# Performance work log

Measured on AMD Instinct MI355X. Metric: run time of the kernel, lower is better.

The kernel has to match this reference:

```python
import jax, jax.numpy as jnp
import numpy as np

N_NODES = 50000
N_EDGES = 800000
DIM = 128


def setup_inputs() -> dict:
    key = jax.random.key(0)
    k_x, k_e, k_w1, k_w2 = jax.random.split(key, 4)
    x = jax.random.normal(k_x, (N_NODES, DIM), dtype=jnp.float32)
    edge_index = jax.random.randint(k_e, (2, N_EDGES), 0, N_NODES, dtype=jnp.int64)
    scale = 1.0 / np.sqrt(DIM)
    W1 = jax.random.normal(k_w1, (DIM, DIM), dtype=jnp.float32) * scale
    b1 = jnp.zeros((DIM,), dtype=jnp.float32)
    W2 = jax.random.normal(k_w2, (DIM, DIM), dtype=jnp.float32) * scale
    b2 = jnp.zeros((DIM,), dtype=jnp.float32)
    return {"x": x, "edge_index": edge_index, "W1": W1, "b1": b1, "W2": W2, "b2": b2}


def _gcn_conv(x, W, b, src, dst, n_nodes):
    """PyG GCNConv: D^{-1/2}(A+I)D^{-1/2} (x @ W) + b, self-loops added."""
    h = x @ W  # [N, D]
    ones = jnp.ones(src.shape[0], dtype=h.dtype)
    # degree of A+I, counting incoming edges at target nodes plus self-loop
    deg = jax.ops.segment_sum(ones, dst, num_segments=n_nodes) + 1.0
    dinv = jax.lax.rsqrt(deg)  # [N]
    norm = dinv[src] * dinv[dst]  # [E]
    msgs = h[src] * norm[:, None]  # [E, D] gather (memory-bound)
    agg = jax.ops.segment_sum(msgs, dst, num_segments=n_nodes)  # scatter-add
    agg = agg + h * (dinv * dinv)[:, None]  # self-loop contribution
    return agg + b


def reference(x, edge_index, W1, b1, W2, b2):
    src, dst = edge_index[0], edge_index[1]
    n = x.shape[0]
    identity = x
    out = jax.nn.relu(_gcn_conv(x, W1, b1, src, dst, n))
    out = _gcn_conv(out, W2, b2, src, dst, n)
    return jax.nn.relu(out + identity)
```

## Files before the change

### kernel.cpp

```cpp
#include <hip/hip_runtime.h>

#define N_NODES 50000
#define N_EDGES 800000
#define DIM 128
#define NB 391
#define CAP 2560
#define NCH 7
#define BIN_CHUNK 4096
#define BIN_BLOCKS 196
#define GEMM_TILES 782
#define AGG_TILES 782
#define NPANEL 4

typedef unsigned int uint;
typedef unsigned short ushort;
typedef __attribute__((ext_vector_type(8))) __bf16 bf16x8;
typedef __attribute__((ext_vector_type(4))) float f32x4;

__device__ __forceinline__ uint f2bf(float f) {
    uint u = __float_as_uint(f);
    return (u + 0x7FFFu + ((u >> 16) & 1u)) >> 16;
}
__device__ __forceinline__ float2 bf2f2(uint u) {
    return make_float2(__uint_as_float(u << 16), __uint_as_float(u & 0xFFFF0000u));
}


__global__ __launch_bounds__(256) void prep_kernel(const float* __restrict__ W1,
                                                   const float* __restrict__ W2,
                                                   uint* __restrict__ Wt1,
                                                   uint* __restrict__ Wt2,
                                                   int* __restrict__ bincursor) {
    int idx = blockIdx.x * 256 + threadIdx.x;
    if (idx < 16384) {
        const float* W = (idx < 8192) ? W1 : W2;
        uint* Wt = (idx < 8192) ? Wt1 : Wt2;
        int i = idx & 8191;
        int n = i >> 6, k2 = i & 63;
        Wt[i] = f2bf(W[(2 * k2) * DIM + n]) | (f2bf(W[(2 * k2 + 1) * DIM + n]) << 16);
    } else {
        int b = idx - 16384;
        if (b < NB) bincursor[b] = b * CAP;
    }
}



__device__ __forceinline__ void gemm_tile64(const float* __restrict__ X,
                                            const uint* __restrict__ Wt, int base,
                                            uint* __restrict__ HP) {
    int t = threadIdx.x;
    int wv = t >> 6;
    int l = t & 63;
    int col = l & 15;
    int g = l >> 4;
    int grow = base + wv * 16 + col;
    int ar = grow > N_NODES - 1 ? N_NODES - 1 : grow;

    bf16x8 af[4];
    const float4* Xr = (const float4*)(X + (size_t)ar * DIM);
#pragma unroll
    for (int kk = 0; kk < 4; ++kk) {
        float4 x0 = Xr[kk * 8 + g * 2];
        float4 x1 = Xr[kk * 8 + g * 2 + 1];
        uint4 p;
        p.x = f2bf(x0.x) | (f2bf(x0.y) << 16);
        p.y = f2bf(x0.z) | (f2bf(x0.w) << 16);
        p.z = f2bf(x1.x) | (f2bf(x1.y) << 16);
        p.w = f2bf(x1.z) | (f2bf(x1.w) << 16);
        af[kk] = __builtin_bit_cast(bf16x8, p);
    }

    const uint4* Wr = (const uint4*)Wt;
    f32x4 acc[8];
#pragma unroll
    for (int n = 0; n < 8; ++n) acc[n] = (f32x4){0.f, 0.f, 0.f, 0.f};

#pragma unroll
    for (int n = 0; n < 8; ++n) {
        const uint4* wrow = Wr + (size_t)(n * 16 + col) * 16;
#pragma unroll
        for (int kk = 0; kk < 4; ++kk) {
            bf16x8 bf = __builtin_bit_cast(bf16x8, wrow[kk * 4 + g]);
            acc[n] = __builtin_amdgcn_mfma_f32_16x16x32_bf16(af[kk], bf, acc[n], 0, 0, 0);
        }
    }

    ushort* Hp = (ushort*)HP;
#pragma unroll
    for (int j = 0; j < 4; ++j) {
        int row = base + wv * 16 + g * 4 + j;
        if (row < N_NODES) {
#pragma unroll
            for (int n = 0; n < 8; ++n) {
                Hp[((size_t)((n >> 1) * N_NODES + row)) * 32 + (n & 1) * 16 + col] =
                    (ushort)f2bf(acc[n][j]);
            }
        }
    }
}


__global__ __launch_bounds__(256) void bin_gemm1_kernel(const int* __restrict__ ei,
                                                        int* __restrict__ bincursor,
                                                        uint* __restrict__ pairs,
                                                        const float* __restrict__ x,
                                                        const uint* __restrict__ Wt1,
                                                        uint* __restrict__ HP) {
    if (blockIdx.x >= BIN_BLOCKS) {
        gemm_tile64(x, Wt1, (blockIdx.x - BIN_BLOCKS) * 64, HP);
        return;
    }
    __shared__ int lh[NB];
    __shared__ int lbase[NB];
    int t = threadIdx.x;
    int eb = blockIdx.x * BIN_CHUNK;

    for (int b = t; b < NB; b += 256) lh[b] = 0;
    __syncthreads();

    int s_reg[16], d_reg[16];
#pragma unroll
    for (int i = 0; i < 16; ++i) {
        int e = eb + i * 256 + t;
        if (e < N_EDGES) {
            s_reg[i] = ei[e];
            d_reg[i] = ei[N_EDGES + e];
            atomicAdd(&lh[d_reg[i] >> 7], 1);
        } else {
            d_reg[i] = -1;
        }
    }
    __syncthreads();

    for (int b = t; b < NB; b += 256) {
        int c = lh[b];
        lbase[b] = c ? atomicAdd(&bincursor[b], c) : 0;
    }
    __syncthreads();
    for (int b = t; b < NB; b += 256) lh[b] = 0;
    __syncthreads();

#pragma unroll
    for (int i = 0; i < 16; ++i) {
        int d = d_reg[i];
        if (d >= 0) {
            int bin = d >> 7;
            int r = atomicAdd(&lh[bin], 1);
            pairs[lbase[bin] + r] = ((uint)s_reg[i] << 7) | (uint)(d & 127);
        }
    }
}


__global__ __launch_bounds__(256) void fill2_kernel(const uint* __restrict__ pairs,
                                                    const int* __restrict__ bincursor,
                                                    int* __restrict__ rowbeg,
                                                    int* __restrict__ rowend,
                                                    float* __restrict__ dinv,
                                                    int* __restrict__ csr_src) {
    __shared__ int cnt[128 * 8];
    __shared__ int nsum[128];
    __shared__ int nbase[128];
    int t = threadIdx.x;
    int blk = blockIdx.x;
    int bs = blk * CAP;
    int be = bincursor[blk];

    for (int i = t; i < 128 * 8; i += 256) cnt[i] = 0;
    __syncthreads();

    for (int p = bs + t; p < be; p += 256) {
        uint pr = pairs[p];
        atomicAdd(&cnt[(pr & 127u) * 8 + (pr >> 20)], 1);
    }
    __syncthreads();

    if (t < 128) {
        int s = 0;
#pragma unroll
        for (int c = 0; c < NCH; ++c) s += cnt[t * 8 + c];
        nsum[t] = s;
        nbase[t] = s;
    }
    __syncthreads();
#pragma unroll
    for (int off = 1; off < 128; off <<= 1) {
        int v = (t < 128 && t >= off) ? nbase[t - off] : 0;
        __syncthreads();
        if (t < 128) nbase[t] += v;
        __syncthreads();
    }

    if (t < 128) {
        int ex = nbase[t] - nsum[t];
        int node = blk * 128 + t;
        if (node < N_NODES) {
            rowbeg[node] = bs + ex;
            rowend[node] = bs + nbase[t];
            dinv[node] = rsqrtf((float)nsum[t] + 1.0f);
        }
        int run = ex;
#pragma unroll
        for (int c = 0; c < NCH; ++c) {
            int v = cnt[t * 8 + c];
            cnt[t * 8 + c] = run;
            run += v;
        }
    }
    __syncthreads();

    for (int p = bs + t; p < be; p += 256) {
        uint pr = pairs[p];
        int r = atomicAdd(&cnt[(pr & 127u) * 8 + (pr >> 20)], 1);
        csr_src[bs + r] = (int)(pr >> 7);
    }
}


template <bool DSRC, bool OBF>
__global__ __launch_bounds__(256) void aggP_kernel(const int* __restrict__ rowbeg,
                                                   const int* __restrict__ rowend,
                                                   const int* __restrict__ csr_src,
                                                   const uint* __restrict__ HP,
                                                   const float* __restrict__ dinv,
                                                   const float* __restrict__ bias,
                                                   const float* __restrict__ resid,
                                                   void* __restrict__ outv) {
    int bid = blockIdx.x;
    int panel = bid & 3;
    int tile = bid >> 2;
    int t = threadIdx.x;
    int wv = t >> 6;
    int l = t & 63;
    int sub = l >> 2;
    int li = l & 3;
    int node = tile * 64 + wv * 16 + sub;
    bool valid = node < N_NODES;
    int nn = valid ? node : N_NODES - 1;

    int beg = rowbeg[nn];
    int end = valid ? rowend[nn] : beg;
    float di = dinv[nn];

    const uint4* H = (const uint4*)HP + (size_t)panel * (N_NODES * 4);

    float a0, a1, a2, a3, a4, a5, a6, a7;
    {
        uint4 su = H[(size_t)nn * 4 + li];
        float2 v0 = bf2f2(su.x), v1 = bf2f2(su.y), v2 = bf2f2(su.z), v3 = bf2f2(su.w);
        float sf = DSRC ? di : 1.0f;
        a0 = sf * v0.x; a1 = sf * v0.y; a2 = sf * v1.x; a3 = sf * v1.y;
        a4 = sf * v2.x; a5 = sf * v2.y; a6 = sf * v3.x; a7 = sf * v3.y;
    }

#define ADDF8(u, f)                                                               \
    {                                                                             \
        float2 v0 = bf2f2(u.x), v1 = bf2f2(u.y), v2 = bf2f2(u.z), v3 = bf2f2(u.w);\
        a0 += f * v0.x; a1 += f * v0.y; a2 += f * v1.x; a3 += f * v1.y;           \
        a4 += f * v2.x; a5 += f * v2.y; a6 += f * v3.x; a7 += f * v3.y;           \
    }

    int e = beg;
    for (; e + 7 < end; e += 8) {
        int s[8];
#pragma unroll
        for (int i = 0; i < 8; ++i) s[i] = csr_src[e + i];
        uint4 u[8];
#pragma unroll
        for (int i = 0; i < 8; ++i) u[i] = H[(size_t)s[i] * 4 + li];
        float f[8];
#pragma unroll
        for (int i = 0; i < 8; ++i) f[i] = DSRC ? dinv[s[i]] : 1.0f;
#pragma unroll
        for (int i = 0; i < 8; ++i) ADDF8(u[i], f[i]);
    }
    if (e + 3 < end) {
        int s[4];
#pragma unroll
        for (int i = 0; i < 4; ++i) s[i] = csr_src[e + i];
        uint4 u[4];
#pragma unroll
        for (int i = 0; i < 4; ++i) u[i] = H[(size_t)s[i] * 4 + li];
        float f[4];
#pragma unroll
        for (int i = 0; i < 4; ++i) f[i] = DSRC ? dinv[s[i]] : 1.0f;
#pragma unroll
        for (int i = 0; i < 4; ++i) ADDF8(u[i], f[i]);
        e += 4;
    }
    for (; e < end; ++e) {
        int s = csr_src[e];
        uint4 u = H[(size_t)s * 4 + li];
        float f = DSRC ? dinv[s] : 1.0f;
        ADDF8(u, f);
    }
#undef ADDF8

    if (!valid) return;

    const float4* B4 = (const float4*)(bias + panel * 32 + li * 8);
    float4 bb0 = B4[0], bb1 = B4[1];
    float r0 = a0 * di + bb0.x, r1 = a1 * di + bb0.y;
    float r2 = a2 * di + bb0.z, r3 = a3 * di + bb0.w;
    float r4 = a4 * di + bb1.x, r5 = a5 * di + bb1.y;
    float r6 = a6 * di + bb1.z, r7 = a7 * di + bb1.w;

    if (OBF) {
        uint4 o;
        o.x = f2bf(fmaxf(r0, 0.f)) | (f2bf(fmaxf(r1, 0.f)) << 16);
        o.y = f2bf(fmaxf(r2, 0.f)) | (f2bf(fmaxf(r3, 0.f)) << 16);
        o.z = f2bf(fmaxf(r4, 0.f)) | (f2bf(fmaxf(r5, 0.f)) << 16);
        o.w = f2bf(fmaxf(r6, 0.f)) | (f2bf(fmaxf(r7, 0.f)) << 16);
        ((uint4*)outv)[(size_t)(panel * N_NODES + node) * 4 + li] = o;
    } else {
        const float4* R4 = (const float4*)(resid + (size_t)node * DIM + panel * 32 + li * 8);
        float4 x0 = R4[0], x1 = R4[1];
        r0 += x0.x; r1 += x0.y; r2 += x0.z; r3 += x0.w;
        r4 += x1.x; r5 += x1.y; r6 += x1.z; r7 += x1.w;
        float4* O4 = (float4*)((float*)outv + (size_t)node * DIM + panel * 32 + li * 8);
        O4[0] = make_float4(fmaxf(r0, 0.f), fmaxf(r1, 0.f), fmaxf(r2, 0.f), fmaxf(r3, 0.f));
        O4[1] = make_float4(fmaxf(r4, 0.f), fmaxf(r5, 0.f), fmaxf(r6, 0.f), fmaxf(r7, 0.f));
    }
}


__global__ __launch_bounds__(256) void gemm2_kernel(const uint* __restrict__ out1P,
                                                    const uint* __restrict__ Wt,
                                                    const float* __restrict__ dinv,
                                                    uint* __restrict__ HP) {
    int t = threadIdx.x;
    int wv = t >> 6;
    int l = t & 63;
    int col = l & 15;
    int g = l >> 4;
    int base = blockIdx.x * 64;
    int grow = base + wv * 16 + col;
    int ar = grow > N_NODES - 1 ? N_NODES - 1 : grow;

    bf16x8 af[4];
#pragma unroll
    for (int kk = 0; kk < 4; ++kk) {
        af[kk] = __builtin_bit_cast(
            bf16x8, *(const uint4*)(out1P + ((size_t)(kk * N_NODES + ar)) * 16 + g * 4));
    }

    const uint4* Wr = (const uint4*)Wt;
    f32x4 acc[8];
#pragma unroll
    for (int n = 0; n < 8; ++n) acc[n] = (f32x4){0.f, 0.f, 0.f, 0.f};

#pragma unroll
    for (int n = 0; n < 8; ++n) {
        const uint4* wrow = Wr + (size_t)(n * 16 + col) * 16;
#pragma unroll
        for (int kk = 0; kk < 4; ++kk) {
            bf16x8 bf = __builtin_bit_cast(bf16x8, wrow[kk * 4 + g]);
            acc[n] = __builtin_amdgcn_mfma_f32_16x16x32_bf16(af[kk], bf, acc[n], 0, 0, 0);
        }
    }

    ushort* Hp = (ushort*)HP;
#pragma unroll
    for (int j = 0; j < 4; ++j) {
        int row = base + wv * 16 + g * 4 + j;
        if (row < N_NODES) {
            float di = dinv[row];
#pragma unroll
            for (int n = 0; n < 8; ++n) {
                Hp[((size_t)((n >> 1) * N_NODES + row)) * 32 + (n & 1) * 16 + col] =
                    (ushort)f2bf(acc[n][j] * di);
            }
        }
    }
}


extern "C" void kernel_launch(void* const* d_in, const int* in_sizes, int n_in,
                              void* d_out, int out_size, void* d_ws, size_t ws_size,
                              hipStream_t stream) {
    const float* x = (const float*)d_in[0];
    const int* edge_index = (const int*)d_in[1];
    const float* W1 = (const float*)d_in[2];
    const float* b1 = (const float*)d_in[3];
    const float* W2 = (const float*)d_in[4];
    const float* b2 = (const float*)d_in[5];
    float* out = (float*)d_out;

    char* ws = (char*)d_ws;
    int*   bincursor = (int*)(ws + 0);
    float* dinv      = (float*)(ws + (64 << 10));
    int*   rowbeg    = (int*)(ws + (320 << 10));
    int*   rowend    = (int*)(ws + (576 << 10));
    int*   csr_src   = (int*)(ws + (1 << 20));
    uint*  pairs     = (uint*)(ws + (6 << 20));
    uint*  HsP       = (uint*)(ws + (11 << 20));
    uint*  out1P     = (uint*)(ws + (24 << 20));
    uint*  Wt1       = (uint*)(ws + (37 << 20));
    uint*  Wt2       = (uint*)(ws + (37 << 20) + (64 << 10));

    prep_kernel<<<66, 256, 0, stream>>>(W1, W2, Wt1, Wt2, bincursor);
    bin_gemm1_kernel<<<BIN_BLOCKS + GEMM_TILES, 256, 0, stream>>>(edge_index, bincursor, pairs,
                                                                  x, Wt1, HsP);
    fill2_kernel<<<NB, 256, 0, stream>>>(pairs, bincursor, rowbeg, rowend, dinv, csr_src);
    aggP_kernel<true, true><<<AGG_TILES * NPANEL, 256, 0, stream>>>(
        rowbeg, rowend, csr_src, HsP, dinv, b1, nullptr, (void*)out1P);
    gemm2_kernel<<<GEMM_TILES, 256, 0, stream>>>(out1P, Wt2, dinv, HsP);
    aggP_kernel<false, false><<<AGG_TILES * NPANEL, 256, 0, stream>>>(
        rowbeg, rowend, csr_src, HsP, dinv, b2, x, (void*)out);
}
```

Before: 140.4 us.

## Use row-major bf16 features, degree-sorted node order, and regrouped kernel fusion

```diff
diff --git a/kernel.cpp b/kernel.cpp
--- a/kernel.cpp
+++ b/kernel.cpp
@@ -8,9 +8,10 @@
 #define NCH 7
 #define BIN_CHUNK 4096
 #define BIN_BLOCKS 196
+#define PREP_BLOCKS 64
 #define GEMM_TILES 782
-#define AGG_TILES 782
-#define NPANEL 4
+#define PERM_SLOTS (NB * 128)
+#define AGG_BLOCKS (PERM_SLOTS / 16)
 
 typedef unsigned int uint;
 typedef unsigned short ushort;
@@ -26,29 +27,67 @@
 }
 
 
-__global__ __launch_bounds__(256) void prep_kernel(const float* __restrict__ W1,
-                                                   const float* __restrict__ W2,
-                                                   uint* __restrict__ Wt1,
-                                                   uint* __restrict__ Wt2,
-                                                   int* __restrict__ bincursor) {
-    int idx = blockIdx.x * 256 + threadIdx.x;
-    if (idx < 16384) {
+__global__ __launch_bounds__(256) void binprep_kernel(const int* __restrict__ ei,
+                                                      int* __restrict__ bincursor,
+                                                      uint* __restrict__ pairs,
+                                                      const float* __restrict__ W1,
+                                                      const float* __restrict__ W2,
+                                                      uint* __restrict__ Wt1,
+                                                      uint* __restrict__ Wt2) {
+    if (blockIdx.x >= BIN_BLOCKS) {
+        int idx = (blockIdx.x - BIN_BLOCKS) * 256 + threadIdx.x;
         const float* W = (idx < 8192) ? W1 : W2;
         uint* Wt = (idx < 8192) ? Wt1 : Wt2;
         int i = idx & 8191;
         int n = i >> 6, k2 = i & 63;
         Wt[i] = f2bf(W[(2 * k2) * DIM + n]) | (f2bf(W[(2 * k2 + 1) * DIM + n]) << 16);
-    } else {
-        int b = idx - 16384;
-        if (b < NB) bincursor[b] = b * CAP;
-    }
-}
-
-
-
-__device__ __forceinline__ void gemm_tile64(const float* __restrict__ X,
-                                            const uint* __restrict__ Wt, int base,
-                                            uint* __restrict__ HP) {
+        return;
+    }
+    __shared__ int lh[NB];
+    __shared__ int lbase[NB];
+    int t = threadIdx.x;
+    int eb = blockIdx.x * BIN_CHUNK;
+
+    for (int b = t; b < NB; b += 256) lh[b] = 0;
+    __syncthreads();
+
+    int s_reg[16], d_reg[16];
+#pragma unroll
+    for (int i = 0; i < 16; ++i) {
+        int e = eb + i * 256 + t;
+        if (e < N_EDGES) {
+            s_reg[i] = ei[e];
+            d_reg[i] = ei[N_EDGES + e];
+            atomicAdd(&lh[d_reg[i] >> 7], 1);
+        } else {
+            d_reg[i] = -1;
+        }
+    }
+    __syncthreads();
+
+    for (int b = t; b < NB; b += 256) {
+        int c = lh[b];
+        lbase[b] = c ? (b * CAP + atomicAdd(&bincursor[b], c)) : 0;
+    }
+    __syncthreads();
+    for (int b = t; b < NB; b += 256) lh[b] = 0;
+    __syncthreads();
+
+#pragma unroll
+    for (int i = 0; i < 16; ++i) {
+        int d = d_reg[i];
+        if (d >= 0) {
+            int bin = d >> 7;
+            int r = atomicAdd(&lh[bin], 1);
+            pairs[lbase[bin] + r] = ((uint)s_reg[i] << 7) | (uint)(d & 127);
+        }
+    }
+}
+
+
+__device__ __forceinline__ void gemm1_tile(const float* __restrict__ X,
+                                           const uint* __restrict__ Wt, int base,
+                                           uint* __restrict__ Hout) {
     int t = threadIdx.x;
     int wv = t >> 6;
     int l = t & 63;
@@ -86,88 +125,44 @@
         }
     }
 
-    ushort* Hp = (ushort*)HP;
 #pragma unroll
     for (int j = 0; j < 4; ++j) {
         int row = base + wv * 16 + g * 4 + j;
         if (row < N_NODES) {
-#pragma unroll
-            for (int n = 0; n < 8; ++n) {
-                Hp[((size_t)((n >> 1) * N_NODES + row)) * 32 + (n & 1) * 16 + col] =
-                    (ushort)f2bf(acc[n][j]);
-            }
-        }
-    }
-}
-
-
-__global__ __launch_bounds__(256) void bin_gemm1_kernel(const int* __restrict__ ei,
-                                                        int* __restrict__ bincursor,
-                                                        uint* __restrict__ pairs,
-                                                        const float* __restrict__ x,
-                                                        const uint* __restrict__ Wt1,
-                                                        uint* __restrict__ HP) {
-    if (blockIdx.x >= BIN_BLOCKS) {
-        gemm_tile64(x, Wt1, (blockIdx.x - BIN_BLOCKS) * 64, HP);
+            ushort* hrow = (ushort*)(Hout + (size_t)row * 64);
+#pragma unroll
+            for (int n = 0; n < 8; ++n) hrow[n * 16 + col] = (ushort)f2bf(acc[n][j]);
+        }
+    }
+}
+
+
+__global__ __launch_bounds__(256) void fillgemm_kernel(const uint* __restrict__ pairs,
+                                                       const int* __restrict__ bincursor,
+                                                       int* __restrict__ rowbeg,
+                                                       int* __restrict__ rowend,
+                                                       float* __restrict__ dinv,
+                                                       int* __restrict__ csr_src,
+                                                       int* __restrict__ nodeperm,
+                                                       const float* __restrict__ x,
+                                                       const uint* __restrict__ Wt1,
+                                                       uint* __restrict__ Hs) {
+    if (blockIdx.x >= NB) {
+        gemm1_tile(x, Wt1, (blockIdx.x - NB) * 64, Hs);
         return;
     }
-    __shared__ int lh[NB];
-    __shared__ int lbase[NB];
-    int t = threadIdx.x;
-    int eb = blockIdx.x * BIN_CHUNK;
-
-    for (int b = t; b < NB; b += 256) lh[b] = 0;
-    __syncthreads();
-
-    int s_reg[16], d_reg[16];
-#pragma unroll
-    for (int i = 0; i < 16; ++i) {
-        int e = eb + i * 256 + t;
-        if (e < N_EDGES) {
-            s_reg[i] = ei[e];
-            d_reg[i] = ei[N_EDGES + e];
-            atomicAdd(&lh[d_reg[i] >> 7], 1);
-        } else {
-            d_reg[i] = -1;
-        }
-    }
-    __syncthreads();
-
-    for (int b = t; b < NB; b += 256) {
-        int c = lh[b];
-        lbase[b] = c ? atomicAdd(&bincursor[b], c) : 0;
-    }
-    __syncthreads();
-    for (int b = t; b < NB; b += 256) lh[b] = 0;
-    __syncthreads();
-
-#pragma unroll
-    for (int i = 0; i < 16; ++i) {
-        int d = d_reg[i];
-        if (d >= 0) {
-            int bin = d >> 7;
-            int r = atomicAdd(&lh[bin], 1);
-            pairs[lbase[bin] + r] = ((uint)s_reg[i] << 7) | (uint)(d & 127);
-        }
-    }
-}
-
-
-__global__ __launch_bounds__(256) void fill2_kernel(const uint* __restrict__ pairs,
-                                                    const int* __restrict__ bincursor,
-                                                    int* __restrict__ rowbeg,
-                                                    int* __restrict__ rowend,
-                                                    float* __restrict__ dinv,
-                                                    int* __restrict__ csr_src) {
     __shared__ int cnt[128 * 8];
     __shared__ int nsum[128];
     __shared__ int nbase[128];
+    __shared__ int dh[64];
+    __shared__ int dcur[64];
     int t = threadIdx.x;
     int blk = blockIdx.x;
     int bs = blk * CAP;
-    int be = bincursor[blk];
+    int be = bs + bincursor[blk];
 
     for (int i = t; i < 128 * 8; i += 256) cnt[i] = 0;
+    if (t < 64) dh[t] = 0;
     __syncthreads();
 
     for (int p = bs + t; p < be; p += 256) {
@@ -192,14 +187,18 @@
         __syncthreads();
     }
 
+    int node = blk * 128 + t;
+    int deg = (t < 128) ? nsum[t] : 0;
     if (t < 128) {
-        int ex = nbase[t] - nsum[t];
-        int node = blk * 128 + t;
+        int ex = nbase[t] - deg;
         if (node < N_NODES) {
             rowbeg[node] = bs + ex;
             rowend[node] = bs + nbase[t];
-            dinv[node] = rsqrtf((float)nsum[t] + 1.0f);
-        }
+            dinv[node] = rsqrtf((float)deg + 1.0f);
+            int db = deg > 63 ? 63 : deg;
+            atomicAdd(&dh[db], 1);
+        }
+        nodeperm[blk * 128 + t] = -1;
         int run = ex;
 #pragma unroll
         for (int c = 0; c < NCH; ++c) {
@@ -210,6 +209,23 @@
     }
     __syncthreads();
 
+    if (t == 0) {
+        int run = 0;
+#pragma unroll
+        for (int i = 0; i < 64; ++i) {
+            int v = dh[i];
+            dcur[i] = run;
+            run += v;
+        }
+    }
+    __syncthreads();
+
+    if (t < 128 && node < N_NODES) {
+        int db = deg > 63 ? 63 : deg;
+        int rk = atomicAdd(&dcur[db], 1);
+        nodeperm[blk * 128 + rk] = node;
+    }
+
     for (int p = bs + t; p < be; p += 256) {
         uint pr = pairs[p];
         int r = atomicAdd(&cnt[(pr & 127u) * 8 + (pr >> 20)], 1);
@@ -219,35 +235,31 @@
 
 
 template <bool DSRC, bool OBF>
-__global__ __launch_bounds__(256) void aggP_kernel(const int* __restrict__ rowbeg,
-                                                   const int* __restrict__ rowend,
-                                                   const int* __restrict__ csr_src,
-                                                   const uint* __restrict__ HP,
-                                                   const float* __restrict__ dinv,
-                                                   const float* __restrict__ bias,
-                                                   const float* __restrict__ resid,
-                                                   void* __restrict__ outv) {
-    int bid = blockIdx.x;
-    int panel = bid & 3;
-    int tile = bid >> 2;
-    int t = threadIdx.x;
-    int wv = t >> 6;
-    int l = t & 63;
-    int sub = l >> 2;
-    int li = l & 3;
-    int node = tile * 64 + wv * 16 + sub;
-    bool valid = node < N_NODES;
-    int nn = valid ? node : N_NODES - 1;
-
-    int beg = rowbeg[nn];
-    int end = valid ? rowend[nn] : beg;
-    float di = dinv[nn];
-
-    const uint4* H = (const uint4*)HP + (size_t)panel * (N_NODES * 4);
-
+__global__ __launch_bounds__(256) void agg_kernel(const int* __restrict__ perm,
+                                                  const int* __restrict__ rowbeg,
+                                                  const int* __restrict__ rowend,
+                                                  const int* __restrict__ csr_src,
+                                                  const uint* __restrict__ Hs,
+                                                  const float* __restrict__ dinv,
+                                                  const float* __restrict__ bias,
+                                                  const float* __restrict__ resid,
+                                                  void* __restrict__ outv) {
+    int gt = blockIdx.x * 256 + threadIdx.x;
+    int wave = gt >> 6;
+    int lane = gt & 63;
+    int grp = lane >> 4;
+    int li = lane & 15;
+    int node = perm[wave * 4 + grp];
+    if (node < 0) return;
+
+    int beg = rowbeg[node];
+    int end = rowend[node];
+    float di = dinv[node];
+
+    const uint4* H4 = (const uint4*)Hs;
     float a0, a1, a2, a3, a4, a5, a6, a7;
     {
-        uint4 su = H[(size_t)nn * 4 + li];
+        uint4 su = H4[(size_t)node * 16 + li];
         float2 v0 = bf2f2(su.x), v1 = bf2f2(su.y), v2 = bf2f2(su.z), v3 = bf2f2(su.w);
         float sf = DSRC ? di : 1.0f;
         a0 = sf * v0.x; a1 = sf * v0.y; a2 = sf * v1.x; a3 = sf * v1.y;
@@ -268,7 +280,7 @@
         for (int i = 0; i < 8; ++i) s[i] = csr_src[e + i];
         uint4 u[8];
 #pragma unroll
-        for (int i = 0; i < 8; ++i) u[i] = H[(size_t)s[i] * 4 + li];
+        for (int i = 0; i < 8; ++i) u[i] = H4[(size_t)s[i] * 16 + li];
         float f[8];
 #pragma unroll
         for (int i = 0; i < 8; ++i) f[i] = DSRC ? dinv[s[i]] : 1.0f;
@@ -281,7 +293,7 @@
         for (int i = 0; i < 4; ++i) s[i] = csr_src[e + i];
         uint4 u[4];
 #pragma unroll
-        for (int i = 0; i < 4; ++i) u[i] = H[(size_t)s[i] * 4 + li];
+        for (int i = 0; i < 4; ++i) u[i] = H4[(size_t)s[i] * 16 + li];
         float f[4];
 #pragma unroll
         for (int i = 0; i < 4; ++i) f[i] = DSRC ? dinv[s[i]] : 1.0f;
@@ -291,16 +303,14 @@
     }
     for (; e < end; ++e) {
         int s = csr_src[e];
-        uint4 u = H[(size_t)s * 4 + li];
+        uint4 u = H4[(size_t)s * 16 + li];
         float f = DSRC ? dinv[s] : 1.0f;
         ADDF8(u, f);
     }
 #undef ADDF8
 
-    if (!valid) return;
-
-    const float4* B4 = (const float4*)(bias + panel * 32 + li * 8);
-    float4 bb0 = B4[0], bb1 = B4[1];
+    const float4* B4 = (const float4*)bias;
+    float4 bb0 = B4[li * 2], bb1 = B4[li * 2 + 1];
     float r0 = a0 * di + bb0.x, r1 = a1 * di + bb0.y;
     float r2 = a2 * di + bb0.z, r3 = a3 * di + bb0.w;
     float r4 = a4 * di + bb1.x, r5 = a5 * di + bb1.y;
@@ -312,23 +322,23 @@
         o.y = f2bf(fmaxf(r2, 0.f)) | (f2bf(fmaxf(r3, 0.f)) << 16);
         o.z = f2bf(fmaxf(r4, 0.f)) | (f2bf(fmaxf(r5, 0.f)) << 16);
         o.w = f2bf(fmaxf(r6, 0.f)) | (f2bf(fmaxf(r7, 0.f)) << 16);
-        ((uint4*)outv)[(size_t)(panel * N_NODES + node) * 4 + li] = o;
+        ((uint4*)outv)[(size_t)node * 16 + li] = o;
     } else {
-        const float4* R4 = (const float4*)(resid + (size_t)node * DIM + panel * 32 + li * 8);
-        float4 x0 = R4[0], x1 = R4[1];
+        const float4* R4 = (const float4*)(resid + (size_t)node * DIM);
+        float4 x0 = R4[li * 2], x1 = R4[li * 2 + 1];
         r0 += x0.x; r1 += x0.y; r2 += x0.z; r3 += x0.w;
         r4 += x1.x; r5 += x1.y; r6 += x1.z; r7 += x1.w;
-        float4* O4 = (float4*)((float*)outv + (size_t)node * DIM + panel * 32 + li * 8);
-        O4[0] = make_float4(fmaxf(r0, 0.f), fmaxf(r1, 0.f), fmaxf(r2, 0.f), fmaxf(r3, 0.f));
-        O4[1] = make_float4(fmaxf(r4, 0.f), fmaxf(r5, 0.f), fmaxf(r6, 0.f), fmaxf(r7, 0.f));
-    }
-}
-
-
-__global__ __launch_bounds__(256) void gemm2_kernel(const uint* __restrict__ out1P,
+        float4* O4 = (float4*)((float*)outv + (size_t)node * DIM);
+        O4[li * 2] = make_float4(fmaxf(r0, 0.f), fmaxf(r1, 0.f), fmaxf(r2, 0.f), fmaxf(r3, 0.f));
+        O4[li * 2 + 1] = make_float4(fmaxf(r4, 0.f), fmaxf(r5, 0.f), fmaxf(r6, 0.f), fmaxf(r7, 0.f));
+    }
+}
+
+
+__global__ __launch_bounds__(256) void gemm2_kernel(const uint* __restrict__ out1b,
                                                     const uint* __restrict__ Wt,
                                                     const float* __restrict__ dinv,
-                                                    uint* __restrict__ HP) {
+                                                    uint* __restrict__ Hout) {
     int t = threadIdx.x;
     int wv = t >> 6;
     int l = t & 63;
@@ -339,11 +349,9 @@
     int ar = grow > N_NODES - 1 ? N_NODES - 1 : grow;
 
     bf16x8 af[4];
-#pragma unroll
-    for (int kk = 0; kk < 4; ++kk) {
-        af[kk] = __builtin_bit_cast(
-            bf16x8, *(const uint4*)(out1P + ((size_t)(kk * N_NODES + ar)) * 16 + g * 4));
-    }
+    const uint4* Xr = (const uint4*)(out1b + (size_t)ar * 64);
+#pragma unroll
+    for (int kk = 0; kk < 4; ++kk) af[kk] = __builtin_bit_cast(bf16x8, Xr[kk * 4 + g]);
 
     const uint4* Wr = (const uint4*)Wt;
     f32x4 acc[8];
@@ -360,17 +368,14 @@
         }
     }
 
-    ushort* Hp = (ushort*)HP;
 #pragma unroll
     for (int j = 0; j < 4; ++j) {
         int row = base + wv * 16 + g * 4 + j;
         if (row < N_NODES) {
             float di = dinv[row];
-#pragma unroll
-            for (int n = 0; n < 8; ++n) {
-                Hp[((size_t)((n >> 1) * N_NODES + row)) * 32 + (n & 1) * 16 + col] =
-                    (ushort)f2bf(acc[n][j] * di);
-            }
+            ushort* hrow = (ushort*)(Hout + (size_t)row * 64);
+#pragma unroll
+            for (int n = 0; n < 8; ++n) hrow[n * 16 + col] = (ushort)f2bf(acc[n][j] * di);
         }
     }
 }
@@ -389,23 +394,25 @@
 
     char* ws = (char*)d_ws;
     int*   bincursor = (int*)(ws + 0);
-    float* dinv      = (float*)(ws + (64 << 10));
-    int*   rowbeg    = (int*)(ws + (320 << 10));
-    int*   rowend    = (int*)(ws + (576 << 10));
-    int*   csr_src   = (int*)(ws + (1 << 20));
+    float* dinv      = (float*)(ws + (256 << 10));
+    int*   rowbeg    = (int*)(ws + (512 << 10));
+    int*   rowend    = (int*)(ws + (768 << 10));
+    int*   nodeperm  = (int*)(ws + (1 << 20));
+    int*   csr_src   = (int*)(ws + (2 << 20));
     uint*  pairs     = (uint*)(ws + (6 << 20));
-    uint*  HsP       = (uint*)(ws + (11 << 20));
-    uint*  out1P     = (uint*)(ws + (24 << 20));
-    uint*  Wt1       = (uint*)(ws + (37 << 20));
-    uint*  Wt2       = (uint*)(ws + (37 << 20) + (64 << 10));
-
-    prep_kernel<<<66, 256, 0, stream>>>(W1, W2, Wt1, Wt2, bincursor);
-    bin_gemm1_kernel<<<BIN_BLOCKS + GEMM_TILES, 256, 0, stream>>>(edge_index, bincursor, pairs,
-                                                                  x, Wt1, HsP);
-    fill2_kernel<<<NB, 256, 0, stream>>>(pairs, bincursor, rowbeg, rowend, dinv, csr_src);
-    aggP_kernel<true, true><<<AGG_TILES * NPANEL, 256, 0, stream>>>(
-        rowbeg, rowend, csr_src, HsP, dinv, b1, nullptr, (void*)out1P);
-    gemm2_kernel<<<GEMM_TILES, 256, 0, stream>>>(out1P, Wt2, dinv, HsP);
-    aggP_kernel<false, false><<<AGG_TILES * NPANEL, 256, 0, stream>>>(
-        rowbeg, rowend, csr_src, HsP, dinv, b2, x, (void*)out);
-}
+    uint*  Hs        = (uint*)(ws + (12 << 20));
+    uint*  out1b     = (uint*)(ws + (25 << 20));
+    uint*  Wt1       = (uint*)(ws + (38 << 20));
+    uint*  Wt2       = (uint*)(ws + (38 << 20) + (64 << 10));
+
+    hipMemsetAsync(bincursor, 0, NB * sizeof(int), stream);
+    binprep_kernel<<<BIN_BLOCKS + PREP_BLOCKS, 256, 0, stream>>>(edge_index, bincursor, pairs,
+                                                                 W1, W2, Wt1, Wt2);
+    fillgemm_kernel<<<NB + GEMM_TILES, 256, 0, stream>>>(pairs, bincursor, rowbeg, rowend, dinv,
+                                                         csr_src, nodeperm, x, Wt1, Hs);
+    agg_kernel<true, true><<<AGG_BLOCKS, 256, 0, stream>>>(nodeperm, rowbeg, rowend, csr_src, Hs,
+                                                           dinv, b1, nullptr, (void*)out1b);
+    gemm2_kernel<<<GEMM_TILES, 256, 0, stream>>>(out1b, Wt2, dinv, Hs);
+    agg_kernel<false, false><<<AGG_BLOCKS, 256, 0, stream>>>(nodeperm, rowbeg, rowend, csr_src,
+                                                             Hs, dinv, b2, x, (void*)out);
+}
```

Result: slower. 153.3 us (+9.2%).
